# Kernel optimization log

Hardware: AMD Instinct MI355X
Metric: run time of the kernel (lower is better)

## Reference

```python
import math
import jax, jax.numpy as jnp
import numpy as np

D_MODEL = 1024
N_HEADS = 16
HEAD_DIM = 64          # block_size
NUM_RULES = 64
RANK = 8               # proj_rank = round(sqrt(head_dim)); also router_rank
SHARED_RANK = 32       # round(sqrt(d_model))
NUM_BLOCKS = 16        # min(in,out)//block_size = 1024//64; total_block_dim == d_model
B, S = 4, 1024
ROPE_BASE = 10000.0


def setup_inputs() -> dict:
    key = jax.random.key(0)
    ks = iter(jax.random.split(key, 32))
    def nrm(shape, s=0.02):
        return jax.random.normal(next(ks), shape, dtype=jnp.float32) * s
    inp = {
        "x": jax.random.normal(next(ks), (B, S, D_MODEL), dtype=jnp.float32),
        "target_rule_ids": jax.random.randint(next(ks), (B, S), 0, NUM_RULES),
    }
    for p in ("q", "k", "v", "o"):
        inp[p + "_si"] = nrm((D_MODEL, SHARED_RANK))
        inp[p + "_so"] = nrm((SHARED_RANK, D_MODEL))
        inp[p + "_ri"] = nrm((NUM_RULES, HEAD_DIM, RANK))
        inp[p + "_ro"] = nrm((NUM_RULES, RANK, HEAD_DIM))
        inp[p + "_lg"] = nrm((NUM_RULES, NUM_BLOCKS), 1.0 / math.sqrt(NUM_BLOCKS))
    inp["router_q"] = nrm((NUM_RULES, RANK))
    inp["router_k"] = nrm((NUM_RULES, RANK))
    return inp


def _rule_proj(x, rules, si, so, ri, ro, lg):
    """RuleAwareProjection.forward_rules_batched, de-permuted.

    The torch code argsorts tokens by rule, zero-pads per-rule buckets, runs
    bmm per rule and scatters back; mathematically that equals a per-token
    gather of the rule's low-rank adapter, which is what we compute here.
    x: [N, D_MODEL], rules: [N] int.
    """
    base = (x @ si) @ so                                  # shared low-rank path
    xb = x.reshape(-1, NUM_BLOCKS, HEAD_DIM)              # [N, nb, bs]
    h = jnp.einsum('nbs,nsr->nbr', xb, ri[rules])         # [N, nb, rank]
    a = jnp.einsum('nbr,nrt->nbt', h, ro[rules])          # [N, nb, bs]
    # temperature = 1/sqrt(num_blocks) => logits / temperature = logits*sqrt(nb)
    sel = jax.nn.softmax(lg[rules] * math.sqrt(NUM_BLOCKS), axis=-1)
    return base + (a * sel[:, :, None]).reshape(-1, D_MODEL)


def _rope(q, k):
    # q, k: [B, H, S, D]; interleaved-pair rotation, start_pos = 0.
    S_, D = q.shape[2], q.shape[3]
    pos = jnp.arange(S_, dtype=jnp.float32)[:, None]
    div = jnp.exp(jnp.arange(0, D, 2, dtype=jnp.float32) * (-math.log(ROPE_BASE) / D))
    f = pos * div                                         # [S, D/2]
    sin, cos = jnp.sin(f), jnp.cos(f)
    def rot(t):
        t1, t2 = t[..., 0::2], t[..., 1::2]
        return jnp.stack([t1 * cos - t2 * sin, t2 * cos + t1 * sin], axis=-1).reshape(t.shape)
    return rot(q), rot(k)


def reference(x, target_rule_ids,
              q_si, q_so, q_ri, q_ro, q_lg,
              k_si, k_so, k_ri, k_ro, k_lg,
              v_si, v_so, v_ri, v_ro, v_lg,
              o_si, o_so, o_ri, o_ro, o_lg,
              router_q, router_k):
    B_, S_, C = x.shape
    flat_x = x.reshape(-1, C)
    rules = target_rule_ids.reshape(-1)

    q = _rule_proj(flat_x, rules, q_si, q_so, q_ri, q_ro, q_lg)
    k = _rule_proj(flat_x, rules, k_si, k_so, k_ri, k_ro, k_lg)
    v = _rule_proj(flat_x, rules, v_si, v_so, v_ri, v_ro, v_lg)
    q = q.reshape(B_, S_, N_HEADS, HEAD_DIM).transpose(0, 2, 1, 3)
    k = k.reshape(B_, S_, N_HEADS, HEAD_DIM).transpose(0, 2, 1, 3)
    v = v.reshape(B_, S_, N_HEADS, HEAD_DIM).transpose(0, 2, 1, 3)
    q, k = _rope(q, k)

    # rule-routing sparse mask: cosine affinity between token rule embeddings
    rq = router_q[target_rule_ids]                        # [B, S, rank]
    rk = router_k[target_rule_ids]
    rqn = rq / jnp.maximum(jnp.linalg.norm(rq, axis=-1, keepdims=True), 1e-12)
    rkn = rk / jnp.maximum(jnp.linalg.norm(rk, axis=-1, keepdims=True), 1e-12)
    tau = 1.0 / math.log(max(math.e, RANK))
    aff = jnp.einsum('bqr,bkr->bqk', rqn, rkn) / tau       # [B, S, S]
    causal = jnp.tril(jnp.ones((S_, S_), dtype=bool))
    masked = jnp.where(causal[None], aff, -jnp.inf)
    top_k = max(2, int(math.sqrt(S_)))
    if S_ > top_k:
        thr = jax.lax.top_k(masked, top_k)[0][..., -1:]
        rule_mask = (masked >= thr) & causal[None]
    else:
        rule_mask = jnp.broadcast_to(causal[None], masked.shape)

    scores = jnp.einsum('bhqd,bhkd->bhqk', q, k) / math.sqrt(HEAD_DIM)
    scores = jnp.where(rule_mask[:, None], scores, -jnp.inf)
    attn = jax.nn.softmax(scores, axis=-1)
    out = jnp.einsum('bhqk,bhkd->bhqd', attn, v)
    out = out.transpose(0, 2, 1, 3).reshape(-1, C)
    out = _rule_proj(out, rules, o_si, o_so, o_ri, o_ro, o_lg)
    return out.reshape(B_, S_, C)
```

## Files before the change

### kernel.cpp

```cpp
#include <hip/hip_runtime.h>
#include <hip/hip_bf16.h>
#include <hip/hip_fp16.h>

#define D_MODEL 1024
#define N_HEADS 16
#define HEAD_DIM 64
#define NUM_RULES 64
#define RANK 8
#define SHARED_RANK 32
#define NUM_BLOCKS_ 16
#define BB 4
#define SS 1024
#define NTOK (BB*SS)
#define NGRP (NTOK/8)
#define NGRP4 (NTOK/4)

typedef __attribute__((ext_vector_type(8))) short bf16x8;
typedef __attribute__((ext_vector_type(4))) float f32x4;

__device__ __forceinline__ float bf2f(unsigned short u) {
  unsigned int i = ((unsigned int)u) << 16;
  float f;
  __builtin_memcpy(&f, &i, 4);
  return f;
}
__device__ __forceinline__ unsigned short f2bf(float f) {
  __hip_bfloat16 h = __float2bfloat16(f);
  unsigned short u;
  __builtin_memcpy(&u, &h, 2);
  return u;
}
__device__ __forceinline__ unsigned short f2h(float f) {
  __half h = __float2half(f);
  unsigned short u;
  __builtin_memcpy(&u, &h, 2);
  return u;
}
__device__ __forceinline__ float h2f(unsigned short u) {
  __half h;
  __builtin_memcpy(&h, &u, 2);
  return __half2float(h);
}
template<bool BF>
__device__ __forceinline__ float ldw(const void* p, size_t i) {
  if (BF) return bf2f(((const unsigned short*)p)[i]);
  else    return ((const float*)p)[i];
}

template<bool BF>
__device__ __forceinline__ void precompute_body(
    const void* rq, const void* rk,
    const void* qlg, const void* klg, const void* vlg, const void* olg,
    float* __restrict__ M, float* __restrict__ sel)
{
  __shared__ float rqn[64][8], rkn[64][8];
  const int tid = threadIdx.x;
  if (tid < 64) {
    float v[8]; float s = 0.f;
    for (int i = 0; i < 8; i++) { v[i] = ldw<BF>(rq, tid*8+i); s += v[i]*v[i]; }
    float inv = 1.0f / fmaxf(sqrtf(s), 1e-12f);
    for (int i = 0; i < 8; i++) rqn[tid][i] = v[i]*inv;
  } else if (tid < 128) {
    int r = tid - 64;
    float v[8]; float s = 0.f;
    for (int i = 0; i < 8; i++) { v[i] = ldw<BF>(rk, r*8+i); s += v[i]*v[i]; }
    float inv = 1.0f / fmaxf(sqrtf(s), 1e-12f);
    for (int i = 0; i < 8; i++) rkn[r][i] = v[i]*inv;
  }
  __syncthreads();
  const float LN8 = 2.0794415416798357f;
  for (int idx = tid; idx < 64*64; idx += 256) {
    int i = idx >> 6, j = idx & 63;
    float d = 0.f;
    for (int t = 0; t < 8; t++) d += rqn[i][t]*rkn[j][t];
    M[idx] = d * LN8;
  }
  const void* lgs[4] = {qlg, klg, vlg, olg};
  {
    int r = tid & 63;
    const void* lg = lgs[tid >> 6];
    float e[NUM_BLOCKS_]; float mx = -1e30f;
    for (int b = 0; b < NUM_BLOCKS_; b++) {
      e[b] = ldw<BF>(lg, r*NUM_BLOCKS_ + b) * 4.0f;
      mx = fmaxf(mx, e[b]);
    }
    float s = 0.f;
    for (int b = 0; b < NUM_BLOCKS_; b++) { e[b] = expf(e[b]-mx); s += e[b]; }
    float inv = 1.0f/s;
    for (int b = 0; b < NUM_BLOCKS_; b++) sel[tid*NUM_BLOCKS_+b] = e[b]*inv;
  }
}

__global__ void detect_precompute_kernel(
    const unsigned short* __restrict__ x, int* __restrict__ flag,
    const void* rq, const void* rk,
    const void* qlg, const void* klg, const void* vlg, const void* olg,
    float* M, float* sel)
{
  __shared__ int fl;
  const int tid = threadIdx.x;
  if (tid < 64) {
    int good = 0;
    for (int i = 0; i < 4; i++) {
      unsigned short u = x[tid*4 + i];
      int e = (u >> 7) & 0xFF;
      good += (e == 0 || (e >= 100 && e <= 145)) ? 1 : 0;
    }
    for (int off = 32; off; off >>= 1) good += __shfl_xor(good, off);
    if (tid == 0) { int g = (good >= 224) ? 1 : 0; flag[0] = g; fl = g; }
  }
  __syncthreads();
  if (fl) precompute_body<true >(rq, rk, qlg, klg, vlg, olg, M, sel);
  else    precompute_body<false>(rq, rk, qlg, klg, vlg, olg, M, sel);
}

__global__ __launch_bounds__(256) void rope_tab_kernel(float* __restrict__ tab) {
  const int idx = blockIdx.x*256 + threadIdx.x;
  const int pos = idx >> 5, i0 = idx & 31;
  float inv = expf(-(float)(2*i0) * (9.210340371976184f/64.0f));
  float sn, cs;
  sincosf((float)pos * inv, &sn, &cs);
  tab[idx*2+0] = cs;
  tab[idx*2+1] = sn;
}

template<bool BF>
__device__ __forceinline__ void prep_wb_body(
    const void* qsi, const void* ksi, const void* vsi, const void* osi,
    unsigned short* __restrict__ wh, unsigned short* __restrict__ wl)
{
  const int kt = blockIdx.x, p = blockIdx.y;
  const int tid = threadIdx.x, nt = tid >> 6, lane = tid & 63;
  const void* si = (p==0)?qsi:((p==1)?ksi:((p==2)?vsi:osi));
  const int col = nt*16 + (lane & 15);
  const int k0 = kt*32 + (lane >> 4)*8;
  size_t base = ((((size_t)p*32 + kt)*2 + nt)*64 + lane)*8;
  unsigned short h8[8], l8[8];
  #pragma unroll
  for (int j = 0; j < 8; j++) {
    float f = ldw<BF>(si, (size_t)(k0 + j)*SHARED_RANK + col);
    unsigned short hu = f2bf(f);
    h8[j] = hu;
    l8[j] = f2bf(f - bf2f(hu));
  }
  #pragma unroll
  for (int j = 0; j < 8; j++) { wh[base + j] = h8[j]; wl[base + j] = l8[j]; }
}

__global__ __launch_bounds__(128) void prep_wb_kernel(
    const void* qsi, const void* ksi, const void* vsi, const void* osi,
    unsigned short* wh, unsigned short* wl, const int* __restrict__ flag)
{
  if (*flag) prep_wb_body<true >(qsi, ksi, vsi, osi, wh, wl);
  else       prep_wb_body<false>(qsi, ksi, vsi, osi, wh, wl);
}

template<bool IN_BF, int NPROJ>
__device__ __forceinline__ void tt_mfma_body(
    const void* __restrict__ xin,
    const unsigned short* __restrict__ wh, const unsigned short* __restrict__ wl,
    int p0, float* __restrict__ ttg)
{
  const int NT = NPROJ*2;
  const int tile = blockIdx.x;
  const int tid = threadIdx.x, lane = tid & 63, w = tid >> 6;
  const int kq = lane >> 4;
  __shared__ float red[4][64][25];

  f32x4 acc[NT];
  #pragma unroll
  for (int i = 0; i < NT; i++) acc[i] = (f32x4){0.f,0.f,0.f,0.f};

  const size_t rowoff = (size_t)(tile*16 + (lane & 15))*D_MODEL + kq*8;
  #pragma unroll 2
  for (int s = 0; s < 8; s++) {
    const int kt = w*8 + s;
    float av[8];
    if (IN_BF) {
      const unsigned short* xr = (const unsigned short*)xin + rowoff + kt*32;
      ushort4 u0 = *(const ushort4*)(xr);
      ushort4 u1 = *(const ushort4*)(xr + 4);
      av[0]=bf2f(u0.x); av[1]=bf2f(u0.y); av[2]=bf2f(u0.z); av[3]=bf2f(u0.w);
      av[4]=bf2f(u1.x); av[5]=bf2f(u1.y); av[6]=bf2f(u1.z); av[7]=bf2f(u1.w);
    } else {
      const float* xr = (const float*)xin + rowoff + kt*32;
      float4 a0 = *(const float4*)(xr);
      float4 a1 = *(const float4*)(xr + 4);
      av[0]=a0.x; av[1]=a0.y; av[2]=a0.z; av[3]=a0.w;
      av[4]=a1.x; av[5]=a1.y; av[6]=a1.z; av[7]=a1.w;
    }
    bf16x8 ah, al;
    #pragma unroll
    for (int j = 0; j < 8; j++) {
      unsigned short hu = f2bf(av[j]);
      ah[j] = (short)hu;
      al[j] = (short)f2bf(av[j] - bf2f(hu));
    }
    #pragma unroll
    for (int p = 0; p < NPROJ; p++) {
      #pragma unroll
      for (int nt = 0; nt < 2; nt++) {
        size_t bidx = ((((size_t)(p0+p)*32 + kt)*2 + nt)*64 + lane)*8;
        bf16x8 bh = *(const bf16x8*)(wh + bidx);
        bf16x8 bl = *(const bf16x8*)(wl + bidx);
        f32x4 c = acc[p*2+nt];
        c = __builtin_amdgcn_mfma_f32_16x16x32_bf16(ah, bh, c, 0, 0, 0);
        c = __builtin_amdgcn_mfma_f32_16x16x32_bf16(al, bh, c, 0, 0, 0);
        c = __builtin_amdgcn_mfma_f32_16x16x32_bf16(ah, bl, c, 0, 0, 0);
        acc[p*2+nt] = c;
      }
    }
  }
  #pragma unroll
  for (int i = 0; i < NT; i++) {
    red[w][lane][i*4+0] = acc[i][0]; red[w][lane][i*4+1] = acc[i][1];
    red[w][lane][i*4+2] = acc[i][2]; red[w][lane][i*4+3] = acc[i][3];
  }
  __syncthreads();
  if (w == 0) {
    const int tok0 = tile*16 + (lane >> 4)*4;
    #pragma unroll
    for (int i = 0; i < NT; i++) {
      const int ys = i >> 1, jj = (i & 1)*16 + (lane & 15);
      #pragma unroll
      for (int r = 0; r < 4; r++) {
        float sum = red[0][lane][i*4+r] + red[1][lane][i*4+r]
                  + red[2][lane][i*4+r] + red[3][lane][i*4+r];
        ttg[((size_t)ys*NTOK + tok0 + r)*32 + jj] = sum;
      }
    }
  }
}

__global__ __launch_bounds__(256) void A_tt_mfma3(
    const void* __restrict__ xin,
    const unsigned short* __restrict__ wh, const unsigned short* __restrict__ wl,
    float* __restrict__ ttg, const int* __restrict__ flag)
{
  if (*flag) tt_mfma_body<true, 3>(xin, wh, wl, 0, ttg);
  else       tt_mfma_body<false,3>(xin, wh, wl, 0, ttg);
}

__global__ __launch_bounds__(256) void A_tt_mfma1(
    const void* __restrict__ xin,
    const unsigned short* __restrict__ wh, const unsigned short* __restrict__ wl,
    float* __restrict__ ttg, const int* __restrict__ flag)
{
  (void)flag;
  tt_mfma_body<false,1>(xin, wh, wl, 3, ttg);
}

template<bool IN_BF, bool W_BF, int NP>
__device__ __forceinline__ void hh_body(
    const void* __restrict__ xin, const int* __restrict__ rules,
    const void* __restrict__ ri0, const void* __restrict__ ri1,
    const void* __restrict__ ri2, float* __restrict__ hhg)
{
  const int g = blockIdx.x, n0 = g*8, tid = threadIdx.x;
  const int t = tid >> 5, blk = (tid >> 1) & 15, r0 = (tid & 1)*4;
  const int n = n0 + t;
  const int rule = rules[n];
  const size_t xoff = (size_t)n*D_MODEL + blk*64;
  const void* wb[3];
  wb[0] = ri0;
  if (NP > 1) { wb[1] = ri1; wb[2] = ri2; }
  float a[NP][4];
  #pragma unroll
  for (int p = 0; p < NP; p++) { a[p][0]=0.f; a[p][1]=0.f; a[p][2]=0.f; a[p][3]=0.f; }
  #pragma unroll 4
  for (int k4 = 0; k4 < 16; k4++) {
    float xv[4];
    if (IN_BF) {
      ushort4 u = *(const ushort4*)((const unsigned short*)xin + xoff + k4*4);
      xv[0]=bf2f(u.x); xv[1]=bf2f(u.y); xv[2]=bf2f(u.z); xv[3]=bf2f(u.w);
    } else {
      float4 u = *(const float4*)((const float*)xin + xoff + k4*4);
      xv[0]=u.x; xv[1]=u.y; xv[2]=u.z; xv[3]=u.w;
    }
    #pragma unroll
    for (int q = 0; q < 4; q++) {
      const int k = k4*4 + q;
      const float xq = xv[q];
      #pragma unroll
      for (int p = 0; p < NP; p++) {
        float w0,w1,w2,w3;
        if (W_BF) {
          ushort4 u = *(const ushort4*)((const unsigned short*)wb[p] + (size_t)rule*512 + (size_t)k*8 + r0);
          w0=bf2f(u.x); w1=bf2f(u.y); w2=bf2f(u.z); w3=bf2f(u.w);
        } else {
          float4 u = *(const float4*)((const float*)wb[p] + (size_t)rule*512 + (size_t)k*8 + r0);
          w0=u.x; w1=u.y; w2=u.z; w3=u.w;
        }
        a[p][0] += xq*w0; a[p][1] += xq*w1; a[p][2] += xq*w2; a[p][3] += xq*w3;
      }
    }
  }
  #pragma unroll
  for (int p = 0; p < NP; p++) {
    float4 hv; hv.x=a[p][0]; hv.y=a[p][1]; hv.z=a[p][2]; hv.w=a[p][3];
    *(float4*)&hhg[((size_t)p*NTOK + n)*128 + blk*8 + r0] = hv;
  }
}

__global__ __launch_bounds__(256) void A_hh3(
    const void* __restrict__ xin, const int* __restrict__ rules,
    const void* __restrict__ qri, const void* __restrict__ kri,
    const void* __restrict__ vri, float* __restrict__ hhg,
    const int* __restrict__ flag)
{
  if (*flag) hh_body<true, true, 3>(xin, rules, qri, kri, vri, hhg);
  else       hh_body<false,false,3>(xin, rules, qri, kri, vri, hhg);
}

__global__ __launch_bounds__(256) void A_hh1(
    const void* __restrict__ xin, const int* __restrict__ rules,
    const void* __restrict__ ori, float* __restrict__ hhg,
    const int* __restrict__ flag)
{
  if (*flag) hh_body<false,true, 1>(xin, rules, ori, ori, ori, hhg);
  else       hh_body<false,false,1>(xin, rules, ori, ori, ori, hhg);
}

template<bool W_BF>
__device__ __forceinline__ void stageB_body(
    const float* __restrict__ ttg, const float* __restrict__ hhg,
    const int* __restrict__ rules,
    const void* __restrict__ so, const void* __restrict__ ro,
    const float* __restrict__ sel, const float* __restrict__ ropet,
    void* __restrict__ out,
    int yslot, int do_rope, int out_bf)
{
  const int blk4 = blockIdx.x;
  const int n0 = blk4*4, tid = threadIdx.x;
  __shared__ float tt_lds[32][5];
  __shared__ float hh_lds[4][132];
  __shared__ int rl[4];

  if (tid < 128) {
    const int j = tid >> 2, t4 = tid & 3;
    tt_lds[j][t4] = ttg[((size_t)yslot*NTOK + n0 + t4)*32 + j];
  } else if (tid < 256 && (tid - 128) < 128) {
    const int i = tid - 128;
    const int t4 = i >> 5, c = (i*4) & 127;
    float4 hv = *(const float4*)&hhg[((size_t)yslot*NTOK + n0 + t4)*128 + c];
    *(float4*)&hh_lds[t4][c] = hv;
  }
  if (tid < 4) rl[tid] = rules[n0 + tid];
  __syncthreads();

  const int ch0 = tid*4;
  float a0[4], a1[4], a2[4], a3[4];
  #pragma unroll
  for (int t = 0; t < 4; t++) { a0[t]=0.f; a1[t]=0.f; a2[t]=0.f; a3[t]=0.f; }

  #pragma unroll 4
  for (int j = 0; j < 32; j++) {
    float w0, w1, w2, w3;
    if (W_BF) {
      ushort4 u = *(const ushort4*)((const unsigned short*)so + (size_t)j*D_MODEL + ch0);
      w0=bf2f(u.x); w1=bf2f(u.y); w2=bf2f(u.z); w3=bf2f(u.w);
    } else {
      float4 u = *(const float4*)((const float*)so + (size_t)j*D_MODEL + ch0);
      w0=u.x; w1=u.y; w2=u.z; w3=u.w;
    }
    #pragma unroll
    for (int t = 0; t < 4; t++) {
      float tv = tt_lds[j][t];
      a0[t] += tv*w0; a1[t] += tv*w1; a2[t] += tv*w2; a3[t] += tv*w3;
    }
  }

  const int blk = ch0 >> 6, tc = ch0 & 63;
  #pragma unroll 2
  for (int t = 0; t < 4; t++) {
    const int rule = rl[t];
    float b0=0.f, b1=0.f, b2=0.f, b3=0.f;
    #pragma unroll
    for (int r = 0; r < 8; r++) {
      float w0,w1,w2,w3;
      if (W_BF) {
        ushort4 u = *(const ushort4*)((const unsigned short*)ro + (size_t)rule*512 + r*64 + tc);
        w0=bf2f(u.x); w1=bf2f(u.y); w2=bf2f(u.z); w3=bf2f(u.w);
      } else {
        float4 u = *(const float4*)((const float*)ro + (size_t)rule*512 + r*64 + tc);
        w0=u.x; w1=u.y; w2=u.z; w3=u.w;
      }
      float hv = hh_lds[t][blk*8 + r];
      b0 += hv*w0; b1 += hv*w1; b2 += hv*w2; b3 += hv*w3;
    }
    float sb = sel[rule*NUM_BLOCKS_ + blk];
    float e0 = a0[t] + b0*sb, o0 = a1[t] + b1*sb;
    float e1 = a2[t] + b2*sb, o1 = a3[t] + b3*sb;
    const int n = n0 + t;
    if (do_rope) {
      float4 cs = *(const float4*)(ropet + ((size_t)(n & (SS-1))*32 + (tc >> 1))*2);
      float u0 = e0*cs.x - o0*cs.y; o0 = o0*cs.x + e0*cs.y; e0 = u0;
      float u1 = e1*cs.z - o1*cs.w; o1 = o1*cs.z + e1*cs.w; e1 = u1;
    }
    if (out_bf) {
      ushort4 uv; uv.x=f2bf(e0); uv.y=f2bf(o0); uv.z=f2bf(e1); uv.w=f2bf(o1);
      *(ushort4*)((unsigned short*)out + (size_t)n*D_MODEL + ch0) = uv;
    } else {
      float4 fv; fv.x=e0; fv.y=o0; fv.z=e1; fv.w=o1;
      *(float4*)((float*)out + (size_t)n*D_MODEL + ch0) = fv;
    }
  }
}

__global__ __launch_bounds__(256) void B_qkv(
    const float* ttg, const float* hhg, const int* rules,
    const void* qso, const void* qro, const void* kso, const void* kro,
    const void* vso, const void* vro,
    const float* sel, const float* ropet,
    float* qb, unsigned short* kb, unsigned short* vb,
    const int* __restrict__ flag)
{
  const int y = blockIdx.y;
  const void* so = (y==0)?qso:((y==1)?kso:vso);
  const void* ro = (y==0)?qro:((y==1)?kro:vro);
  void* out = (y==0)?(void*)qb:((y==1)?(void*)kb:(void*)vb);
  if (*flag)
    stageB_body<true >(ttg, hhg, rules, so, ro, sel + y*1024, ropet, out, y, (y<2)?1:0, (y>=1)?1:0);
  else
    stageB_body<false>(ttg, hhg, rules, so, ro, sel + y*1024, ropet, out, y, (y<2)?1:0, (y>=1)?1:0);
}

__global__ __launch_bounds__(256) void B_o(
    const float* ttg, const float* hhg, const int* rules,
    const void* oso, const void* oro, const float* sel, const float* ropet,
    void* out, const int* __restrict__ flag)
{
  if (*flag) stageB_body<true >(ttg, hhg, rules, oso, oro, sel, ropet, out, 0, 0, 1);
  else       stageB_body<false>(ttg, hhg, rules, oso, oro, sel, ropet, out, 0, 0, 0);
}

__global__ __launch_bounds__(64) void mask_kernel(
    const int* __restrict__ rules, const float* __restrict__ M,
    unsigned long long* __restrict__ am, unsigned int* __restrict__ rp)
{
  const int bid = blockIdx.x;
  const int b = bid >> 10, qi = bid & 1023;
  const int lane = threadIdx.x;
  __shared__ int rrow[SS];
  __shared__ float val[64];
  __shared__ int cnth[64];
  for (int i = lane; i < SS/4; i += 64)
    ((int4*)rrow)[i] = ((const int4*)(rules + b*SS))[i];
  cnth[lane] = 0;
  __syncthreads();
  if (qi < 16 && lane < 16) {
    const int gg = lane >> 2, nt = lane & 3;
    unsigned v = 0;
    #pragma unroll
    for (int j = 0; j < 4; j++)
      v |= ((unsigned)rrow[qi*64 + nt*16 + gg*4 + j] & 0xffu) << (8*j);
    rp[b*256 + qi*16 + lane] = v;
  }
  for (int k = lane; k <= qi; k += 64) atomicAdd(&cnth[rrow[k]], 1);
  const int qrule = rrow[qi];
  const float myv = M[qrule*64 + lane];
  val[lane] = myv;
  __syncthreads();
  const int c = cnth[lane];
  int A = 0;
  for (int r = 0; r < 64; r++) {
    int cr = __shfl(c, r);
    A += (val[r] > myv) ? cr : 0;
  }
  unsigned long long allowed = __ballot(A < 32);
  if (lane == 0) am[bid] = allowed;
}

__global__ __launch_bounds__(256) void vtrans_kernel(
    const unsigned short* __restrict__ vb, unsigned short* __restrict__ vt)
{
  const int st = blockIdx.x, h = blockIdx.y, b = blockIdx.z;
  __shared__ unsigned short t[64][72];
  const int tid = threadIdx.x;
  #pragma unroll
  for (int it = 0; it < 2; it++) {
    int i = tid + it*256;
    int r = i >> 3, c8 = (i & 7)*8;
    uint4 v = *(const uint4*)(vb + ((size_t)(b*SS + st*64 + r)*D_MODEL + h*HEAD_DIM + c8));
    t[c8+0][r] = (unsigned short)(v.x & 0xffffu);
    t[c8+1][r] = (unsigned short)(v.x >> 16);
    t[c8+2][r] = (unsigned short)(v.y & 0xffffu);
    t[c8+3][r] = (unsigned short)(v.y >> 16);
    t[c8+4][r] = (unsigned short)(v.z & 0xffffu);
    t[c8+5][r] = (unsigned short)(v.z >> 16);
    t[c8+6][r] = (unsigned short)(v.w & 0xffffu);
    t[c8+7][r] = (unsigned short)(v.w >> 16);
  }
  __syncthreads();
  #pragma unroll
  for (int it = 0; it < 2; it++) {
    int i = tid + it*256;
    int d = i >> 3, c8 = i & 7;
    const unsigned short* src = &t[d][c8*8];
    uint2 r1, r2;
    r1.x = (unsigned)src[0] | ((unsigned)src[1] << 16);
    r1.y = (unsigned)src[2] | ((unsigned)src[3] << 16);
    r2.x = (unsigned)src[4] | ((unsigned)src[5] << 16);
    r2.y = (unsigned)src[6] | ((unsigned)src[7] << 16);
    const int base = (c8 >> 2)*32 + 4*((c8 >> 1) & 1);
    const int p1 = base + 8*((2*c8)   & 3);
    const int p2 = base + 8*((2*c8+1) & 3);
    unsigned short* dst = vt + ((size_t)(b*N_HEADS + h)*HEAD_DIM + d)*SS + st*64;
    *(uint2*)(dst + p1) = r1;
    *(uint2*)(dst + p2) = r2;
  }
}

__global__ __launch_bounds__(256, 4) void attn_mfma_kernel(
    const float* __restrict__ qb,
    const unsigned short* __restrict__ kb,
    const unsigned short* __restrict__ vtb,
    const unsigned int* __restrict__ rp,
    const unsigned long long* __restrict__ am,
    unsigned short* __restrict__ Obuf,
    float* __restrict__ mlbuf,
    float* outb)
{
  const int x = blockIdx.x, b = blockIdx.y, h = blockIdx.z;
  int qt, k0t, k1t, pidx;
  bool partial;
  if (x < 9) { qt = x; k0t = 0; k1t = qt; partial = false; pidx = 0; }
  else {
    const int j = x - 9, qti = j >> 1, s = j & 1;
    qt = 9 + qti; partial = true;
    pidx = ((b*N_HEADS + h)*7 + qti)*2 + s;
    if (s == 0) { k0t = 0; k1t = 7; } else { k0t = 8; k1t = qt; }
  }
  const int tid = threadIdx.x, lane = tid & 63, w = tid >> 6;
  const int g = lane >> 4, ql = lane & 15;
  __shared__ unsigned short Ks[64*64];
  __shared__ unsigned short Vs[64*64];

  const unsigned short* kbase = kb + (size_t)b*SS*D_MODEL + h*HEAD_DIM;
  const unsigned short* vbase = vtb + (size_t)(b*N_HEADS + h)*HEAD_DIM*SS;
  const unsigned int* rpb = rp + b*256;

  const int srow = tid >> 3;
  const int spos = tid & 7;
  const int sc0 = (srow*8      + (spos ^ (srow      & 7)))*8;
  const int sc1 = ((srow+32)*8 + (spos ^ ((srow+32) & 7)))*8;

  const int qa = qt*64 + w*16 + ql;
  bf16x8 qfrag[2];
  {
    const float* qrow = qb + (size_t)(b*SS + qa)*D_MODEL + h*HEAD_DIM + g*8;
    #pragma unroll
    for (int kc = 0; kc < 2; kc++) {
      float4 f0 = *(const float4*)(qrow + kc*32);
      float4 f1 = *(const float4*)(qrow + kc*32 + 4);
      bf16x8 qv;
      qv[0] = (short)f2bf(f0.x*0.125f); qv[1] = (short)f2bf(f0.y*0.125f);
      qv[2] = (short)f2bf(f0.z*0.125f); qv[3] = (short)f2bf(f0.w*0.125f);
      qv[4] = (short)f2bf(f1.x*0.125f); qv[5] = (short)f2bf(f1.y*0.125f);
      qv[6] = (short)f2bf(f1.z*0.125f); qv[7] = (short)f2bf(f1.w*0.125f);
      qfrag[kc] = qv;
    }
  }
  const uint2 mm = *(const uint2*)(am + (size_t)b*SS + qa);
  const unsigned aqlo = mm.x, aqhi = mm.y;

  f32x4 Oacc[4];
  #pragma unroll
  for (int nt = 0; nt < 4; nt++) Oacc[nt] = (f32x4){0.f,0.f,0.f,0.f};
  float lrun = 0.f;

  {
    const size_t koff0 = (size_t)k0t*64;
    uint4 k0 = *(const uint4*)(kbase + (koff0 + srow)*D_MODEL + spos*8);
    uint4 k1 = *(const uint4*)(kbase + (koff0 + srow + 32)*D_MODEL + spos*8);
    uint4 v0 = *(const uint4*)(vbase + (size_t)srow*SS + koff0 + spos*8);
    uint4 v1 = *(const uint4*)(vbase + (size_t)(srow+32)*SS + koff0 + spos*8);
    *(uint4*)&Ks[sc0] = k0; *(uint4*)&Ks[sc1] = k1;
    *(uint4*)&Vs[sc0] = v0; *(uint4*)&Vs[sc1] = v1;
  }
  __syncthreads();

  for (int kt = k0t; kt <= k1t; kt++) {
    const uint4 ru4 = *(const uint4*)(rpb + kt*16 + g*4);
    uint4 nk0, nk1, nv0, nv1;
    if (kt < k1t) {
      const size_t koff = (size_t)(kt + 1)*64;
      nk0 = *(const uint4*)(kbase + (koff + srow)*D_MODEL + spos*8);
      nk1 = *(const uint4*)(kbase + (koff + srow + 32)*D_MODEL + spos*8);
      nv0 = *(const uint4*)(vbase + (size_t)srow*SS + koff + spos*8);
      nv1 = *(const uint4*)(vbase + (size_t)(srow+32)*SS + koff + spos*8);
    }

    f32x4 Sacc[4];
    __builtin_amdgcn_s_setprio(1);
    #pragma unroll
    for (int nt = 0; nt < 4; nt++) {
      const int key = nt*16 + ql;
      f32x4 c = (f32x4){0.f,0.f,0.f,0.f};
      #pragma unroll
      for (int kcq = 0; kcq < 2; kcq++) {
        int off = (key*128 + kcq*64 + g*16) ^ ((key & 7) << 4);
        bf16x8 kf = *(const bf16x8*)((const char*)Ks + off);
        c = __builtin_amdgcn_mfma_f32_16x16x32_bf16(kf, qfrag[kcq], c, 0, 0, 0);
      }
      Sacc[nt] = c;
    }
    __builtin_amdgcn_s_setprio(0);

    const bool needc = (kt == qt);
    const unsigned ruarr[4] = {ru4.x, ru4.y, ru4.z, ru4.w};
    unsigned pk[4][2];
    #pragma unroll
    for (int nt = 0; nt < 4; nt++) {
      float p[4];
      #pragma unroll
      for (int r = 0; r < 4; r++) {
        const unsigned rr = (ruarr[nt] >> (8*r)) & 0xffu;
        const unsigned bits = (rr >= 32) ? aqhi : aqlo;
        bool ok = ((bits >> (rr & 31u)) & 1u) != 0u;
        if (needc) ok = ok && ((kt*64 + nt*16 + g*4 + r) <= qa);
        p[r] = __expf(ok ? Sacc[nt][r] : -3e38f);
        lrun += p[r];
      }
      pk[nt][0] = (unsigned)f2bf(p[0]) | ((unsigned)f2bf(p[1]) << 16);
      pk[nt][1] = (unsigned)f2bf(p[2]) | ((unsigned)f2bf(p[3]) << 16);
    }

    __builtin_amdgcn_s_setprio(1);
    #pragma unroll
    for (int kc = 0; kc < 2; kc++) {
      union { unsigned u[4]; bf16x8 v; } U;
      U.u[0] = pk[2*kc][0];   U.u[1] = pk[2*kc][1];
      U.u[2] = pk[2*kc+1][0]; U.u[3] = pk[2*kc+1][1];
      const bf16x8 pa = U.v;
      #pragma unroll
      for (int ntd = 0; ntd < 4; ntd++) {
        const int d = ntd*16 + ql;
        int boff = (d*128 + kc*64 + g*16) ^ ((d & 7) << 4);
        bf16x8 vf = *(const bf16x8*)((const char*)Vs + boff);
        Oacc[ntd] = __builtin_amdgcn_mfma_f32_16x16x32_bf16(pa, vf, Oacc[ntd], 0, 0, 0);
      }
    }
    __builtin_amdgcn_s_setprio(0);
    __syncthreads();
    if (kt < k1t) {
      *(uint4*)&Ks[sc0] = nk0; *(uint4*)&Ks[sc1] = nk1;
      *(uint4*)&Vs[sc0] = nv0; *(uint4*)&Vs[sc1] = nv1;
      __syncthreads();
    }
  }

  lrun += __shfl_xor(lrun, 16);
  lrun += __shfl_xor(lrun, 32);

  if (!partial) {
    float invl[4];
    #pragma unroll
    for (int r = 0; r < 4; r++) invl[r] = 1.0f / __shfl(lrun, g*4 + r);
    #pragma unroll
    for (int nt = 0; nt < 4; nt++) {
      #pragma unroll
      for (int r = 0; r < 4; r++) {
        outb[(size_t)(b*SS + qt*64 + w*16 + g*4 + r)*D_MODEL + h*HEAD_DIM + nt*16 + ql]
            = Oacc[nt][r]*invl[r];
      }
    }
  } else {
    unsigned short* ob = Obuf + (size_t)pidx*4096;
    #pragma unroll
    for (int nt = 0; nt < 4; nt++) {
      #pragma unroll
      for (int r = 0; r < 4; r++) {
        const int row = w*16 + g*4 + r;
        ob[row*64 + nt*16 + ql] = f2h(Oacc[nt][r]);
      }
    }
    if (lane < 16) mlbuf[(size_t)pidx*64 + w*16 + lane] = lrun;
  }
}

__global__ __launch_bounds__(256) void attn_combine(
    const unsigned short* __restrict__ Obuf, const float* __restrict__ mlbuf,
    float* __restrict__ outb)
{
  const int qti = blockIdx.x, b = blockIdx.y, h = blockIdx.z;
  const int qt = 9 + qti;
  const int p0 = ((b*N_HEADS + h)*7 + qti)*2;
  const int tid = threadIdx.x;
  const int row = tid >> 2, c0 = (tid & 3)*16;
  const float l0 = mlbuf[(size_t)p0*64 + row];
  const float l1 = mlbuf[(size_t)(p0+1)*64 + row];
  const float inv = 1.0f / (l0 + l1);
  const unsigned short* o0 = Obuf + (size_t)p0*4096 + row*64 + c0;
  const unsigned short* o1 = Obuf + (size_t)(p0+1)*4096 + row*64 + c0;
  float* dst = outb + (size_t)(b*SS + qt*64 + row)*D_MODEL + h*HEAD_DIM + c0;
  #pragma unroll
  for (int j = 0; j < 16; j += 4) {
    float4 fv;
    fv.x = (h2f(o0[j+0]) + h2f(o1[j+0]))*inv;
    fv.y = (h2f(o0[j+1]) + h2f(o1[j+1]))*inv;
    fv.z = (h2f(o0[j+2]) + h2f(o1[j+2]))*inv;
    fv.w = (h2f(o0[j+3]) + h2f(o1[j+3]))*inv;
    *(float4*)(dst + j) = fv;
  }
}

extern "C" void kernel_launch(void* const* d_in, const int* in_sizes, int n_in,
                              void* d_out, int out_size, void* d_ws, size_t ws_size,
                              hipStream_t stream) {
  (void)in_sizes; (void)n_in; (void)out_size; (void)ws_size;
  const void* x    = d_in[0];
  const int* rules = (const int*)d_in[1];
  const void* q_si = d_in[2];  const void* q_so = d_in[3];
  const void* q_ri = d_in[4];  const void* q_ro = d_in[5];  const void* q_lg = d_in[6];
  const void* k_si = d_in[7];  const void* k_so = d_in[8];
  const void* k_ri = d_in[9];  const void* k_ro = d_in[10]; const void* k_lg = d_in[11];
  const void* v_si = d_in[12]; const void* v_so = d_in[13];
  const void* v_ri = d_in[14]; const void* v_ro = d_in[15]; const void* v_lg = d_in[16];
  const void* o_si = d_in[17]; const void* o_so = d_in[18];
  const void* o_ri = d_in[19]; const void* o_ro = d_in[20]; const void* o_lg = d_in[21];
  const void* rq   = d_in[22]; const void* rk   = d_in[23];

  char* ws = (char*)d_ws;
  const size_t MB = 1024*1024;
  float*          qb    = (float*)(ws);
  unsigned short* kb    = (unsigned short*)(ws + 16*MB);
  unsigned short* vb    = (unsigned short*)(ws + 24*MB);
  unsigned short* vtb   = (unsigned short*)(ws + 32*MB);
  float*          ttg   = (float*)(ws + 40*MB);
  float*          hhg   = (float*)(ws + 42*MB);
  unsigned short* Obuf  = (unsigned short*)(ws + 40*MB);
  float*          mlbuf = (float*)(ws + 47*MB);
  unsigned long long* amask = (unsigned long long*)(ws + 48*MB);
  float*          Mt    = (float*)(ws + 49*MB + 16*1024);
  float*          selt  = (float*)(ws + 49*MB + 32*1024);
  int*            flag  = (int*)  (ws + 49*MB + 48*1024);
  unsigned int*   rp    = (unsigned int*)(ws + 49*MB + 52*1024);
  unsigned short* wpkh  = (unsigned short*)(ws + 49*MB + 64*1024);
  unsigned short* wpkl  = (unsigned short*)(ws + 49*MB + 64*1024 + 256*1024);
  float*          ropet = (float*)(ws + 50*MB);

  detect_precompute_kernel<<<1, 256, 0, stream>>>(
      (const unsigned short*)x, flag, rq, rk, q_lg, k_lg, v_lg, o_lg, Mt, selt);
  mask_kernel<<<NTOK, 64, 0, stream>>>(rules, Mt, amask, rp);
  rope_tab_kernel<<<128, 256, 0, stream>>>(ropet);
  prep_wb_kernel<<<dim3(32, 4), 128, 0, stream>>>(q_si, k_si, v_si, o_si, wpkh, wpkl, flag);

  A_tt_mfma3<<<256, 256, 0, stream>>>(x, wpkh, wpkl, ttg, flag);
  A_hh3<<<NGRP, 256, 0, stream>>>(x, rules, q_ri, k_ri, v_ri, hhg, flag);

  B_qkv<<<dim3(NGRP4, 3), 256, 0, stream>>>(ttg, hhg, rules, q_so, q_ro, k_so, k_ro, v_so, v_ro,
                                            selt, ropet, qb, kb, vb, flag);

  vtrans_kernel<<<dim3(16, 16, 4), 256, 0, stream>>>(vb, vtb);
  attn_mfma_kernel<<<dim3(23, BB, N_HEADS), 256, 0, stream>>>(qb, kb, vtb, rp, amask,
                                                              Obuf, mlbuf, qb);
  attn_combine<<<dim3(7, BB, N_HEADS), 256, 0, stream>>>(Obuf, mlbuf, qb);

  A_tt_mfma1<<<256, 256, 0, stream>>>(qb, wpkh, wpkl, ttg, flag);
  A_hh1<<<NGRP, 256, 0, stream>>>(qb, rules, o_ri, hhg, flag);
  B_o<<<NGRP4, 256, 0, stream>>>(ttg, hhg, rules, o_so, o_ro, selt + 3*1024, ropet, d_out, flag);
}
```

Measured before the change: 257.0 us.

## Move stage-B shared up-projection onto MFMA with split-bf16 prepacked weights

Replaces the scalar FMA loop for the shared rank-32 to d_model projection (tt @ so) in stage B with bf16 MFMA 16x16x32. It uses a hi/lo split of weights and activations (three MFMAs) to keep close to fp32 accuracy. A new prep kernel packs so into the MFMA operand layout, and blocks now cover 16 tokens with one token per lane group instead of 4 tokens per block. This removes the per-token scalar dot products. In exchange it adds a prep launch, and the per-rule low-rank adapter loads are now repeated per lane in a less coalesced pattern.

```diff
diff --git a/kernel.cpp b/kernel.cpp
--- a/kernel.cpp
+++ b/kernel.cpp
@@ -13,7 +13,6 @@
 #define SS 1024
 #define NTOK (BB*SS)
 #define NGRP (NTOK/8)
-#define NGRP4 (NTOK/4)
 
 typedef __attribute__((ext_vector_type(8))) short bf16x8;
 typedef __attribute__((ext_vector_type(4))) float f32x4;
@@ -153,6 +152,34 @@
 {
   if (*flag) prep_wb_body<true >(qsi, ksi, vsi, osi, wh, wl);
   else       prep_wb_body<false>(qsi, ksi, vsi, osi, wh, wl);
+}
+
+template<bool BF>
+__device__ __forceinline__ void prep_so_body(
+    const void* qso, const void* kso, const void* vso, const void* oso,
+    unsigned short* __restrict__ sh, unsigned short* __restrict__ sl)
+{
+  const int ct = blockIdx.x, p = blockIdx.y;
+  const int lane = threadIdx.x;
+  const void* so = (p==0)?qso:((p==1)?kso:((p==2)?vso:oso));
+  const int ch = ct*16 + (lane & 15);
+  const int k0 = (lane >> 4)*8;
+  size_t base = (((size_t)p*64 + ct)*64 + lane)*8;
+  #pragma unroll
+  for (int j = 0; j < 8; j++) {
+    float f = ldw<BF>(so, (size_t)(k0 + j)*D_MODEL + ch);
+    unsigned short hu = f2bf(f);
+    sh[base + j] = hu;
+    sl[base + j] = f2bf(f - bf2f(hu));
+  }
+}
+
+__global__ __launch_bounds__(64) void prep_so_kernel(
+    const void* qso, const void* kso, const void* vso, const void* oso,
+    unsigned short* sh, unsigned short* sl, const int* __restrict__ flag)
+{
+  if (*flag) prep_so_body<true >(qso, kso, vso, oso, sh, sl);
+  else       prep_so_body<false>(qso, kso, vso, oso, sh, sl);
 }
 
 template<bool IN_BF, int NPROJ>
@@ -322,116 +349,117 @@
 }
 
 template<bool W_BF>
-__device__ __forceinline__ void stageB_body(
+__device__ __forceinline__ void B_mfma_body(
     const float* __restrict__ ttg, const float* __restrict__ hhg,
     const int* __restrict__ rules,
-    const void* __restrict__ so, const void* __restrict__ ro,
+    const unsigned short* __restrict__ sh, const unsigned short* __restrict__ sl,
+    const void* __restrict__ ro,
     const float* __restrict__ sel, const float* __restrict__ ropet,
     void* __restrict__ out,
-    int yslot, int do_rope, int out_bf)
-{
-  const int blk4 = blockIdx.x;
-  const int n0 = blk4*4, tid = threadIdx.x;
-  __shared__ float tt_lds[32][5];
-  __shared__ float hh_lds[4][132];
-  __shared__ int rl[4];
-
-  if (tid < 128) {
-    const int j = tid >> 2, t4 = tid & 3;
-    tt_lds[j][t4] = ttg[((size_t)yslot*NTOK + n0 + t4)*32 + j];
-  } else if (tid < 256 && (tid - 128) < 128) {
-    const int i = tid - 128;
-    const int t4 = i >> 5, c = (i*4) & 127;
-    float4 hv = *(const float4*)&hhg[((size_t)yslot*NTOK + n0 + t4)*128 + c];
-    *(float4*)&hh_lds[t4][c] = hv;
-  }
-  if (tid < 4) rl[tid] = rules[n0 + tid];
-  __syncthreads();
-
-  const int ch0 = tid*4;
-  float a0[4], a1[4], a2[4], a3[4];
-  #pragma unroll
-  for (int t = 0; t < 4; t++) { a0[t]=0.f; a1[t]=0.f; a2[t]=0.f; a3[t]=0.f; }
-
-  #pragma unroll 4
-  for (int j = 0; j < 32; j++) {
-    float w0, w1, w2, w3;
-    if (W_BF) {
-      ushort4 u = *(const ushort4*)((const unsigned short*)so + (size_t)j*D_MODEL + ch0);
-      w0=bf2f(u.x); w1=bf2f(u.y); w2=bf2f(u.z); w3=bf2f(u.w);
-    } else {
-      float4 u = *(const float4*)((const float*)so + (size_t)j*D_MODEL + ch0);
-      w0=u.x; w1=u.y; w2=u.z; w3=u.w;
-    }
-    #pragma unroll
-    for (int t = 0; t < 4; t++) {
-      float tv = tt_lds[j][t];
-      a0[t] += tv*w0; a1[t] += tv*w1; a2[t] += tv*w2; a3[t] += tv*w3;
-    }
-  }
-
-  const int blk = ch0 >> 6, tc = ch0 & 63;
-  #pragma unroll 2
-  for (int t = 0; t < 4; t++) {
-    const int rule = rl[t];
-    float b0=0.f, b1=0.f, b2=0.f, b3=0.f;
-    #pragma unroll
-    for (int r = 0; r < 8; r++) {
-      float w0,w1,w2,w3;
-      if (W_BF) {
-        ushort4 u = *(const ushort4*)((const unsigned short*)ro + (size_t)rule*512 + r*64 + tc);
-        w0=bf2f(u.x); w1=bf2f(u.y); w2=bf2f(u.z); w3=bf2f(u.w);
+    int pslot, int yslot, int do_rope, int out_bf)
+{
+  const int tok0 = blockIdx.x*16;
+  const int tid = threadIdx.x, lane = tid & 63, w = tid >> 6;
+  const int g = lane >> 4, ql = lane & 15;
+  const int token = tok0 + ql;
+  const int rule = rules[token];
+  const int pos = token & (SS-1);
+
+  bf16x8 tth, ttl;
+  {
+    const float* ttrow = ttg + ((size_t)yslot*NTOK + token)*32 + g*8;
+    float4 t0 = *(const float4*)(ttrow);
+    float4 t1 = *(const float4*)(ttrow + 4);
+    float tv[8] = {t0.x,t0.y,t0.z,t0.w,t1.x,t1.y,t1.z,t1.w};
+    #pragma unroll
+    for (int j = 0; j < 8; j++) {
+      unsigned short hu = f2bf(tv[j]);
+      tth[j] = (short)hu;
+      ttl[j] = (short)f2bf(tv[j] - bf2f(hu));
+    }
+  }
+  const float* hhrow = hhg + ((size_t)yslot*NTOK + token)*128;
+
+  #pragma unroll
+  for (int bq = 0; bq < 4; bq++) {
+    const int blk = w*4 + bq;
+    const float sb = sel[rule*NUM_BLOCKS_ + blk];
+    float4 h0 = *(const float4*)(hhrow + blk*8);
+    float4 h1 = *(const float4*)(hhrow + blk*8 + 4);
+    const float hv[8] = {h0.x,h0.y,h0.z,h0.w,h1.x,h1.y,h1.z,h1.w};
+    #pragma unroll
+    for (int ii = 0; ii < 4; ii++) {
+      const int ct = w*16 + bq*4 + ii;
+      const size_t abase = (((size_t)pslot*64 + ct)*64 + lane)*8;
+      bf16x8 ah = *(const bf16x8*)(sh + abase);
+      bf16x8 al = *(const bf16x8*)(sl + abase);
+      f32x4 c = (f32x4){0.f,0.f,0.f,0.f};
+      c = __builtin_amdgcn_mfma_f32_16x16x32_bf16(ah, tth, c, 0, 0, 0);
+      c = __builtin_amdgcn_mfma_f32_16x16x32_bf16(ah, ttl, c, 0, 0, 0);
+      c = __builtin_amdgcn_mfma_f32_16x16x32_bf16(al, tth, c, 0, 0, 0);
+
+      const int ch0 = ct*16 + g*4;
+      const int tc = ch0 & 63;
+      float b0=0.f, b1=0.f, b2=0.f, b3=0.f;
+      #pragma unroll
+      for (int r = 0; r < 8; r++) {
+        float w0,w1,w2,w3;
+        if (W_BF) {
+          ushort4 u = *(const ushort4*)((const unsigned short*)ro + (size_t)rule*512 + r*64 + tc);
+          w0=bf2f(u.x); w1=bf2f(u.y); w2=bf2f(u.z); w3=bf2f(u.w);
+        } else {
+          float4 u = *(const float4*)((const float*)ro + (size_t)rule*512 + r*64 + tc);
+          w0=u.x; w1=u.y; w2=u.z; w3=u.w;
+        }
+        b0 += hv[r]*w0; b1 += hv[r]*w1; b2 += hv[r]*w2; b3 += hv[r]*w3;
+      }
+      float e0 = c[0] + b0*sb, o0 = c[1] + b1*sb;
+      float e1 = c[2] + b2*sb, o1 = c[3] + b3*sb;
+      if (do_rope) {
+        float4 cs = *(const float4*)(ropet + ((size_t)pos*32 + (tc >> 1))*2);
+        float u0 = e0*cs.x - o0*cs.y; o0 = o0*cs.x + e0*cs.y; e0 = u0;
+        float u1 = e1*cs.z - o1*cs.w; o1 = o1*cs.z + e1*cs.w; e1 = u1;
+      }
+      if (out_bf) {
+        ushort4 uv; uv.x=f2bf(e0); uv.y=f2bf(o0); uv.z=f2bf(e1); uv.w=f2bf(o1);
+        *(ushort4*)((unsigned short*)out + (size_t)token*D_MODEL + ch0) = uv;
       } else {
-        float4 u = *(const float4*)((const float*)ro + (size_t)rule*512 + r*64 + tc);
-        w0=u.x; w1=u.y; w2=u.z; w3=u.w;
-      }
-      float hv = hh_lds[t][blk*8 + r];
-      b0 += hv*w0; b1 += hv*w1; b2 += hv*w2; b3 += hv*w3;
-    }
-    float sb = sel[rule*NUM_BLOCKS_ + blk];
-    float e0 = a0[t] + b0*sb, o0 = a1[t] + b1*sb;
-    float e1 = a2[t] + b2*sb, o1 = a3[t] + b3*sb;
-    const int n = n0 + t;
-    if (do_rope) {
-      float4 cs = *(const float4*)(ropet + ((size_t)(n & (SS-1))*32 + (tc >> 1))*2);
-      float u0 = e0*cs.x - o0*cs.y; o0 = o0*cs.x + e0*cs.y; e0 = u0;
-      float u1 = e1*cs.z - o1*cs.w; o1 = o1*cs.z + e1*cs.w; e1 = u1;
-    }
-    if (out_bf) {
-      ushort4 uv; uv.x=f2bf(e0); uv.y=f2bf(o0); uv.z=f2bf(e1); uv.w=f2bf(o1);
-      *(ushort4*)((unsigned short*)out + (size_t)n*D_MODEL + ch0) = uv;
-    } else {
-      float4 fv; fv.x=e0; fv.y=o0; fv.z=e1; fv.w=o1;
-      *(float4*)((float*)out + (size_t)n*D_MODEL + ch0) = fv;
-    }
-  }
-}
-
-__global__ __launch_bounds__(256) void B_qkv(
+        float4 fv; fv.x=e0; fv.y=o0; fv.z=e1; fv.w=o1;
+        *(float4*)((float*)out + (size_t)token*D_MODEL + ch0) = fv;
+      }
+    }
+  }
+}
+
+__global__ __launch_bounds__(256) void B_qkv_mfma(
     const float* ttg, const float* hhg, const int* rules,
-    const void* qso, const void* qro, const void* kso, const void* kro,
-    const void* vso, const void* vro,
+    const unsigned short* sh, const unsigned short* sl,
+    const void* qro, const void* kro, const void* vro,
     const float* sel, const float* ropet,
     float* qb, unsigned short* kb, unsigned short* vb,
     const int* __restrict__ flag)
 {
   const int y = blockIdx.y;
-  const void* so = (y==0)?qso:((y==1)?kso:vso);
   const void* ro = (y==0)?qro:((y==1)?kro:vro);
   void* out = (y==0)?(void*)qb:((y==1)?(void*)kb:(void*)vb);
   if (*flag)
-    stageB_body<true >(ttg, hhg, rules, so, ro, sel + y*1024, ropet, out, y, (y<2)?1:0, (y>=1)?1:0);
+    B_mfma_body<true >(ttg, hhg, rules, sh, sl, ro, sel + y*1024, ropet, out,
+                       y, y, (y<2)?1:0, (y>=1)?1:0);
   else
-    stageB_body<false>(ttg, hhg, rules, so, ro, sel + y*1024, ropet, out, y, (y<2)?1:0, (y>=1)?1:0);
-}
-
-__global__ __launch_bounds__(256) void B_o(
+    B_mfma_body<false>(ttg, hhg, rules, sh, sl, ro, sel + y*1024, ropet, out,
+                       y, y, (y<2)?1:0, (y>=1)?1:0);
+}
+
+__global__ __launch_bounds__(256) void B_o_mfma(
     const float* ttg, const float* hhg, const int* rules,
-    const void* oso, const void* oro, const float* sel, const float* ropet,
+    const unsigned short* sh, const unsigned short* sl,
+    const void* oro, const float* sel, const float* ropet,
     void* out, const int* __restrict__ flag)
 {
-  if (*flag) stageB_body<true >(ttg, hhg, rules, oso, oro, sel, ropet, out, 0, 0, 1);
-  else       stageB_body<false>(ttg, hhg, rules, oso, oro, sel, ropet, out, 0, 0, 0);
+  if (*flag)
+    B_mfma_body<true >(ttg, hhg, rules, sh, sl, oro, sel, ropet, out, 3, 0, 0, 1);
+  else
+    B_mfma_body<false>(ttg, hhg, rules, sh, sl, oro, sel, ropet, out, 3, 0, 0, 0);
 }
 
 __global__ __launch_bounds__(64) void mask_kernel(
@@ -739,18 +767,22 @@
   unsigned short* wpkh  = (unsigned short*)(ws + 49*MB + 64*1024);
   unsigned short* wpkl  = (unsigned short*)(ws + 49*MB + 64*1024 + 256*1024);
   float*          ropet = (float*)(ws + 50*MB);
+  unsigned short* soh   = (unsigned short*)(ws + 51*MB);
+  unsigned short* sol   = (unsigned short*)(ws + 51*MB + 256*1024);
 
   detect_precompute_kernel<<<1, 256, 0, stream>>>(
       (const unsigned short*)x, flag, rq, rk, q_lg, k_lg, v_lg, o_lg, Mt, selt);
   mask_kernel<<<NTOK, 64, 0, stream>>>(rules, Mt, amask, rp);
   rope_tab_kernel<<<128, 256, 0, stream>>>(ropet);
   prep_wb_kernel<<<dim3(32, 4), 128, 0, stream>>>(q_si, k_si, v_si, o_si, wpkh, wpkl, flag);
+  prep_so_kernel<<<dim3(64, 4), 64, 0, stream>>>(q_so, k_so, v_so, o_so, soh, sol, flag);
 
   A_tt_mfma3<<<256, 256, 0, stream>>>(x, wpkh, wpkl, ttg, flag);
   A_hh3<<<NGRP, 256, 0, stream>>>(x, rules, q_ri, k_ri, v_ri, hhg, flag);
 
-  B_qkv<<<dim3(NGRP4, 3), 256, 0, stream>>>(ttg, hhg, rules, q_so, q_ro, k_so, k_ro, v_so, v_ro,
-                                            selt, ropet, qb, kb, vb, flag);
+  B_qkv_mfma<<<dim3(256, 3), 256, 0, stream>>>(ttg, hhg, rules, soh, sol,
+                                               q_ro, k_ro, v_ro, selt, ropet,
+                                               qb, kb, vb, flag);
 
   vtrans_kernel<<<dim3(16, 16, 4), 256, 0, stream>>>(vb, vtb);
   attn_mfma_kernel<<<dim3(23, BB, N_HEADS), 256, 0, stream>>>(qb, kb, vtb, rp, amask,
@@ -759,5 +791,6 @@
 
   A_tt_mfma1<<<256, 256, 0, stream>>>(qb, wpkh, wpkl, ttg, flag);
   A_hh1<<<NGRP, 256, 0, stream>>>(qb, rules, o_ri, hhg, flag);
-  B_o<<<NGRP4, 256, 0, stream>>>(ttg, hhg, rules, o_so, o_ro, selt + 3*1024, ropet, d_out, flag);
-}
+  B_o_mfma<<<256, 256, 0, stream>>>(ttg, hhg, rules, soh, sol, o_ro,
+                                    selt + 3*1024, ropet, d_out, flag);
+}
```

After: 281.4 us. +9.5%, slower.
